# Optimization experiments

Measured on AMD Instinct MI355X. Metric: run time of the kernel, lower is better.

Reference implementation:

```python
import jax, jax.numpy as jnp
import numpy as np

B = 2048
DIMS = [4096, 8192, 8192, 4096]
SPARSITY = 1e-4


def setup_inputs() -> dict:
    key = jax.random.key(0)
    ks = jax.random.split(key, 10)
    x = jax.random.normal(ks[0], (B, DIMS[0]), dtype=jnp.float32)
    inp = {"x": x}
    for i in range(3):
        fan_in, fan_out = DIMS[i], DIMS[i + 1]
        # xavier_uniform_ for tanh
        limit = float(np.sqrt(6.0 / (fan_in + fan_out)))
        W = jax.random.uniform(ks[1 + 3 * i], (fan_out, fan_in),
                               dtype=jnp.float32, minval=-limit, maxval=limit)
        b = jax.random.uniform(ks[2 + 3 * i], (fan_out,), dtype=jnp.float32,
                               minval=-1.0 / np.sqrt(fan_in), maxval=1.0 / np.sqrt(fan_in))
        m = jax.random.bernoulli(ks[3 + 3 * i], p=SPARSITY, shape=(fan_out, fan_in))
        inp[f"W{i+1}"] = W
        inp[f"b{i+1}"] = b
        inp[f"m{i+1}"] = m
    return inp


def reference(x, W1, b1, m1, W2, b2, m2, W3, b3, m3):
    # Each layer: mask weight, dense linear (y = x @ (W*m)^T + b), tanh except last.
    h = jnp.tanh(x @ (W1 * m1).T + b1)        # [B, 8192]
    h = jnp.tanh(h @ (W2 * m2).T + b2)        # [B, 8192]
    out = h @ (W3 * m3).T + b3                # [B, 4096]
    return out
```

## Files before the change

### kernel.cpp

```cpp
#include <hip/hip_runtime.h>
#include <hip/hip_bf16.h>
#include <stdint.h>

#define CAP 32

static constexpr int BATCH = 2048;
static constexpr int D0 = 4096;
static constexpr int D1 = 8192;
static constexpr int D2 = 8192;
static constexpr int D3 = 4096;
static constexpr int ROWS_PAD = 8192;

static constexpr size_t PREFIX_BYTES = 16u << 20;

static constexpr size_t OFF_DET   = 0;
static constexpr size_t OFF_CNT   = 256;
static constexpr size_t OFF_REFD  = OFF_CNT + 3ull*ROWS_PAD*4;
static constexpr size_t OFF_XNEED = OFF_REFD + 2ull*ROWS_PAD*4;
static constexpr size_t ZERO_BYTES= OFF_XNEED + (size_t)D0*4;
static constexpr size_t OFF_TB    = ZERO_BYTES;
static constexpr size_t OFF_RK    = OFF_TB + 2ull*ROWS_PAD*4;
static constexpr size_t OFF_RW    = OFF_RK + 3ull*ROWS_PAD*CAP*4;
static constexpr size_t OFF_XT    = OFF_RW + 3ull*ROWS_PAD*CAP*4;
static constexpr size_t OFF_H1    = OFF_XT + 33554432ull;
static constexpr size_t OFF_H2    = OFF_H1 + 67108864ull;
static constexpr size_t WS_BIG    = OFF_H2 + 67108864ull;

__global__ void detect_kernel(const uint8_t* __restrict__ m, unsigned* __restrict__ det) {
    const uint4* p = (const uint4*)m;
    const int n16 = (int)(PREFIX_BYTES / 16);
    unsigned c123 = 0, c4 = 0;
    for (int i = blockIdx.x * blockDim.x + threadIdx.x; i < n16; i += gridDim.x * blockDim.x) {
        uint4 q = p[i];
        if ((q.x | q.y | q.z | q.w) == 0u) continue;
        unsigned w[4] = {q.x, q.y, q.z, q.w};
        for (int t = 0; t < 4; ++t) {
            unsigned v = w[t];
            if (!v) continue;
            for (int bb = 0; bb < 4; ++bb) {
                if ((v >> (8 * bb)) & 0xFFu) {
                    int posmod8 = ((t * 4 + bb) & 7);
                    if (posmod8 & 3) c123++;
                    else if (posmod8 == 4) c4++;
                }
            }
        }
    }
    if (c123) atomicAdd(&det[0], c123);
    if (c4)   atomicAdd(&det[1], c4);
}

__device__ __forceinline__ int decide_mode(const unsigned* det) {
    unsigned c123 = det[0], c4 = det[1];
    if (c123 > 1050u) return 0;
    if (c123 > 400u)  return 1;
    return (c4 > 80u) ? 1 : 2;
}

__device__ __forceinline__ void extract_row(const void* mask, const float* W,
                                            int fan_in, int row, int mode,
                                            int* cnt, int* rowk, float* roww,
                                            int* refd_prev) {
    __shared__ int lcnt;
    __shared__ int lk[CAP];
    if (threadIdx.x == 0) lcnt = 0;
    __syncthreads();

    auto push = [&](int k) {
        int pos = atomicAdd(&lcnt, 1);
        if (pos < CAP) lk[pos] = k;
    };

    if (mode == 0) {
        const uint4* p = (const uint4*)((const uint8_t*)mask + (size_t)row * fan_in);
        const int nch = fan_in / 16;
        for (int ci = threadIdx.x; ci < nch; ci += blockDim.x) {
            uint4 q = p[ci];
            if ((q.x | q.y | q.z | q.w) == 0u) continue;
            unsigned w[4] = {q.x, q.y, q.z, q.w};
            int base = ci * 16;
            for (int t = 0; t < 4; ++t) {
                unsigned v = w[t];
                if (!v) continue;
                for (int bb = 0; bb < 4; ++bb)
                    if ((v >> (8 * bb)) & 0xFFu) push(base + t * 4 + bb);
            }
        }
    } else if (mode == 1) {
        const int4* p = (const int4*)((const int*)mask + (size_t)row * fan_in);
        const int nch = fan_in / 4;
        for (int ci = threadIdx.x; ci < nch; ci += blockDim.x) {
            int4 q = p[ci];
            if ((q.x | q.y | q.z | q.w) == 0) continue;
            int base = ci * 4;
            if (q.x) push(base + 0);
            if (q.y) push(base + 1);
            if (q.z) push(base + 2);
            if (q.w) push(base + 3);
        }
    } else {
        const longlong2* p = (const longlong2*)((const long long*)mask + (size_t)row * fan_in);
        const int nch = fan_in / 2;
        for (int ci = threadIdx.x; ci < nch; ci += blockDim.x) {
            longlong2 q = p[ci];
            if ((q.x | q.y) == 0ll) continue;
            int base = ci * 2;
            if (q.x) push(base + 0);
            if (q.y) push(base + 1);
        }
    }
    __syncthreads();

    if (threadIdx.x == 0) {
        int c = lcnt;
        if (c > CAP) c = CAP;
        for (int a = 1; a < c; ++a) {
            int v = lk[a];
            int b = a - 1;
            while (b >= 0 && lk[b] > v) { lk[b + 1] = lk[b]; --b; }
            lk[b + 1] = v;
        }
        cnt[row] = c;
        for (int a = 0; a < c; ++a) {
            int k = lk[a];
            rowk[(size_t)row * CAP + a] = k;
            roww[(size_t)row * CAP + a] = W[(size_t)row * fan_in + k];
            if (refd_prev) atomicOr(&refd_prev[k], 1);
        }
    }
}

__global__ void extract_all_kernel(const void* __restrict__ m1, const float* __restrict__ W1,
                                   const void* __restrict__ m2, const float* __restrict__ W2,
                                   const void* __restrict__ m3, const float* __restrict__ W3,
                                   const float* __restrict__ b1, const float* __restrict__ b2,
                                   const unsigned* __restrict__ det,
                                   int* __restrict__ cnt1, int* __restrict__ cnt2, int* __restrict__ cnt3,
                                   int* __restrict__ rk1, int* __restrict__ rk2, int* __restrict__ rk3,
                                   float* __restrict__ rw1, float* __restrict__ rw2, float* __restrict__ rw3,
                                   int* __restrict__ refd1, int* __restrict__ refd2,
                                   int* __restrict__ xneed,
                                   float* __restrict__ tb1, float* __restrict__ tb2) {
    const int bid = blockIdx.x;
    const int mode = decide_mode(det);
    if (bid < D1) {
        extract_row(m1, W1, D0, bid, mode, cnt1, rk1, rw1, xneed);
    } else if (bid < D1 + D2) {
        extract_row(m2, W2, D1, bid - D1, mode, cnt2, rk2, rw2, refd1);
    } else if (bid < D1 + D2 + D3) {
        extract_row(m3, W3, D2, bid - D1 - D2, mode, cnt3, rk3, rw3, refd2);
    } else {
        int tid = (bid - (D1 + D2 + D3)) * 256 + threadIdx.x;
        if (tid < D1) tb1[tid] = tanhf(b1[tid]);
        else if (tid < D1 + D2) tb2[tid - D1] = tanhf(b2[tid - D1]);
    }
}

__global__ void transpose_x_kernel(const float* __restrict__ in, float* __restrict__ out,
                                   const int* __restrict__ xneed) {
    __shared__ float tile[32][33];
    int c0 = blockIdx.x * 32, r0 = blockIdx.y * 32;
    for (int i = threadIdx.y; i < 32; i += 8)
        tile[i][threadIdx.x] = in[(size_t)(r0 + i) * D0 + c0 + threadIdx.x];
    __syncthreads();
    for (int i = threadIdx.y; i < 32; i += 8)
        if (xneed[c0 + i])
            out[(size_t)(c0 + i) * BATCH + r0 + threadIdx.x] = tile[threadIdx.x][i];
}

template<bool HAS_TB>
__global__ void layer_kernel(const float* __restrict__ inT,
                             const float* __restrict__ bias,
                             const float* __restrict__ tb_in,
                             const int* __restrict__ cnt_in,
                             const int* __restrict__ cnt,
                             const int* __restrict__ rowk,
                             const float* __restrict__ roww,
                             const int* __restrict__ refd,
                             float* __restrict__ outT) {
    const int j = blockIdx.x;
    const int c = cnt[j];
    if (c == 0 || refd[j] == 0) return;

    const int*   kk = rowk + (size_t)j * CAP;
    const float* ww = roww + (size_t)j * CAP;

    float base = bias[j];
    if (HAS_TB) {
        for (int e = 0; e < c; ++e) {
            int k = kk[e];
            if (cnt_in[k] == 0) base += ww[e] * tb_in[k];
        }
    }

    const int l = threadIdx.x;
    float4 acc0 = make_float4(base, base, base, base);
    float4 acc1 = acc0;

    for (int e = 0; e < c; ++e) {
        int k = kk[e];
        if (HAS_TB && cnt_in[k] == 0) continue;
        const float w = ww[e];
        const float* row = inT + (size_t)k * BATCH;
        float4 v0 = *(const float4*)(row + l * 4);
        float4 v1 = *(const float4*)(row + 1024 + l * 4);
        acc0.x += w * v0.x; acc0.y += w * v0.y; acc0.z += w * v0.z; acc0.w += w * v0.w;
        acc1.x += w * v1.x; acc1.y += w * v1.y; acc1.z += w * v1.z; acc1.w += w * v1.w;
    }

    acc0.x = tanhf(acc0.x); acc0.y = tanhf(acc0.y);
    acc0.z = tanhf(acc0.z); acc0.w = tanhf(acc0.w);
    acc1.x = tanhf(acc1.x); acc1.y = tanhf(acc1.y);
    acc1.z = tanhf(acc1.z); acc1.w = tanhf(acc1.w);

    float* orow = outT + (size_t)j * BATCH;
    *(float4*)(orow + l * 4) = acc0;
    *(float4*)(orow + 1024 + l * 4) = acc1;
}

__global__ void l3t_kernel(const float* __restrict__ h2T,
                           const float* __restrict__ b3, const float* __restrict__ tb2,
                           const int* __restrict__ cnt2,
                           const int* __restrict__ c3, const int* __restrict__ k3,
                           const float* __restrict__ w3,
                           float* __restrict__ out) {
    __shared__ float tile[32][33];
    const int j0 = blockIdx.x * 32, b0 = blockIdx.y * 32;
    const int tx = threadIdx.x, ty = threadIdx.y;

    for (int s = 0; s < 4; ++s) {
        int jl = ty + 8 * s;
        int j = j0 + jl;
        float acc = b3[j];
        int c = c3[j];
        const int* kk = k3 + (size_t)j * CAP;
        const float* ww = w3 + (size_t)j * CAP;
        for (int e = 0; e < c; ++e) {
            int k = kk[e];
            float w = ww[e];
            acc += w * (cnt2[k] ? h2T[(size_t)k * BATCH + b0 + tx] : tb2[k]);
        }
        tile[jl][tx] = acc;
    }
    __syncthreads();
    for (int s = 0; s < 4; ++s) {
        int bl = ty + 8 * s;
        out[(size_t)(b0 + bl) * D3 + j0 + tx] = tile[tx][bl];
    }
}

__global__ void out_kernel(const float* __restrict__ x,
                           const float* __restrict__ b1, const float* __restrict__ b2,
                           const float* __restrict__ b3,
                           const int* __restrict__ c1, const int* __restrict__ k1,
                           const float* __restrict__ w1,
                           const int* __restrict__ c2, const int* __restrict__ k2,
                           const float* __restrict__ w2,
                           const int* __restrict__ c3, const int* __restrict__ k3,
                           const float* __restrict__ w3,
                           float* __restrict__ out) {
    int idx = blockIdx.x * blockDim.x + threadIdx.x;
    if (idx >= BATCH * D3) return;
    int b = idx >> 12;
    int j = idx & 4095;

    float acc = b3[j];
    int c = c3[j];
    for (int e = 0; e < c; ++e) {
        int kk2 = k3[(size_t)j * CAP + e];
        float a2 = b2[kk2];
        int cc2 = c2[kk2];
        for (int e2 = 0; e2 < cc2; ++e2) {
            int kk1 = k2[(size_t)kk2 * CAP + e2];
            float a1 = b1[kk1];
            int cc1 = c1[kk1];
            for (int e1 = 0; e1 < cc1; ++e1) {
                int kk0 = k1[(size_t)kk1 * CAP + e1];
                a1 += w1[(size_t)kk1 * CAP + e1] * x[(size_t)b * D0 + kk0];
            }
            a2 += w2[(size_t)kk2 * CAP + e2] * tanhf(a1);
        }
        acc += w3[(size_t)j * CAP + e] * tanhf(a2);
    }
    out[idx] = acc;
}

extern "C" void kernel_launch(void* const* d_in, const int* in_sizes, int n_in,
                              void* d_out, int out_size, void* d_ws, size_t ws_size,
                              hipStream_t stream) {
    const float* x  = (const float*)d_in[0];
    const float* W1 = (const float*)d_in[1];
    const float* b1 = (const float*)d_in[2];
    const void*  m1 = d_in[3];
    const float* W2 = (const float*)d_in[4];
    const float* b2 = (const float*)d_in[5];
    const void*  m2 = d_in[6];
    const float* W3 = (const float*)d_in[7];
    const float* b3 = (const float*)d_in[8];
    const void*  m3 = d_in[9];

    uint8_t* ws = (uint8_t*)d_ws;
    unsigned* det = (unsigned*)(ws + OFF_DET);
    int* cnt1 = (int*)(ws + OFF_CNT);
    int* cnt2 = cnt1 + ROWS_PAD;
    int* cnt3 = cnt2 + ROWS_PAD;
    int* refd1 = (int*)(ws + OFF_REFD);
    int* refd2 = refd1 + ROWS_PAD;
    int* xneed = (int*)(ws + OFF_XNEED);
    float* tb1 = (float*)(ws + OFF_TB);
    float* tb2 = tb1 + ROWS_PAD;
    int* rk1 = (int*)(ws + OFF_RK);
    int* rk2 = rk1 + (size_t)ROWS_PAD * CAP;
    int* rk3 = rk2 + (size_t)ROWS_PAD * CAP;
    float* rw1 = (float*)(ws + OFF_RW);
    float* rw2 = rw1 + (size_t)ROWS_PAD * CAP;
    float* rw3 = rw2 + (size_t)ROWS_PAD * CAP;
    float* xT  = (float*)(ws + OFF_XT);
    float* h1T = (float*)(ws + OFF_H1);
    float* h2T = (float*)(ws + OFF_H2);

    hipMemsetAsync(ws, 0, ZERO_BYTES, stream);

    detect_kernel<<<1024, 256, 0, stream>>>((const uint8_t*)m1, det);

    const int EX_BLOCKS = D1 + D2 + D3 + (D1 + D2) / 256;
    extract_all_kernel<<<EX_BLOCKS, 256, 0, stream>>>(
        m1, W1, m2, W2, m3, W3, b1, b2, det,
        cnt1, cnt2, cnt3, rk1, rk2, rk3, rw1, rw2, rw3,
        refd1, refd2, xneed, tb1, tb2);

    if (ws_size >= WS_BIG) {
        transpose_x_kernel<<<dim3(D0 / 32, BATCH / 32), dim3(32, 8), 0, stream>>>(x, xT, xneed);

        layer_kernel<false><<<D1, 256, 0, stream>>>(
            xT, b1, nullptr, nullptr, cnt1, rk1, rw1, refd1, h1T);
        layer_kernel<true><<<D2, 256, 0, stream>>>(
            h1T, b2, tb1, cnt1, cnt2, rk2, rw2, refd2, h2T);
        l3t_kernel<<<dim3(D3 / 32, BATCH / 32), dim3(32, 8), 0, stream>>>(
            h2T, b3, tb2, cnt2, cnt3, rk3, rw3, (float*)d_out);
    } else {
        out_kernel<<<(BATCH * D3 + 255) / 256, 256, 0, stream>>>(
            x, b1, b2, b3,
            cnt1, rk1, rw1,
            cnt2, rk2, rw2,
            cnt3, rk3, rw3,
            (float*)d_out);
    }
}
```

Before: 190.2 us.

## Fuse mask extraction with x transpose and layer-1 compute across kernels

Restructures the launch schedule so layer-1 mask extraction runs in the same kernel as the x transpose, and layer-2/3 extraction runs alongside the layer-1 sparse matmul. This overlaps independent stages and removes a kernel launch. It also drops the refd1/xneed liveness filtering, so all of x is transposed and all layer-1 rows are computed. That adds extra work in exchange for fewer stage barriers, and it shrinks the memset region.

After: 191.2 us. About the same (+0.6%).

```diff
diff --git a/kernel.cpp b/kernel.cpp
--- a/kernel.cpp
+++ b/kernel.cpp
@@ -14,11 +14,10 @@
 static constexpr size_t PREFIX_BYTES = 16u << 20;
 
 static constexpr size_t OFF_DET   = 0;
-static constexpr size_t OFF_CNT   = 256;
-static constexpr size_t OFF_REFD  = OFF_CNT + 3ull*ROWS_PAD*4;
-static constexpr size_t OFF_XNEED = OFF_REFD + 2ull*ROWS_PAD*4;
-static constexpr size_t ZERO_BYTES= OFF_XNEED + (size_t)D0*4;
-static constexpr size_t OFF_TB    = ZERO_BYTES;
+static constexpr size_t OFF_REFD2 = 256;
+static constexpr size_t ZERO_BYTES= OFF_REFD2 + (size_t)ROWS_PAD*4;
+static constexpr size_t OFF_CNT   = ZERO_BYTES;
+static constexpr size_t OFF_TB    = OFF_CNT + 3ull*ROWS_PAD*4;
 static constexpr size_t OFF_RK    = OFF_TB + 2ull*ROWS_PAD*4;
 static constexpr size_t OFF_RW    = OFF_RK + 3ull*ROWS_PAD*CAP*4;
 static constexpr size_t OFF_XT    = OFF_RW + 3ull*ROWS_PAD*CAP*4;
@@ -130,57 +129,19 @@
     }
 }
 
-__global__ void extract_all_kernel(const void* __restrict__ m1, const float* __restrict__ W1,
-                                   const void* __restrict__ m2, const float* __restrict__ W2,
-                                   const void* __restrict__ m3, const float* __restrict__ W3,
-                                   const float* __restrict__ b1, const float* __restrict__ b2,
-                                   const unsigned* __restrict__ det,
-                                   int* __restrict__ cnt1, int* __restrict__ cnt2, int* __restrict__ cnt3,
-                                   int* __restrict__ rk1, int* __restrict__ rk2, int* __restrict__ rk3,
-                                   float* __restrict__ rw1, float* __restrict__ rw2, float* __restrict__ rw3,
-                                   int* __restrict__ refd1, int* __restrict__ refd2,
-                                   int* __restrict__ xneed,
-                                   float* __restrict__ tb1, float* __restrict__ tb2) {
-    const int bid = blockIdx.x;
-    const int mode = decide_mode(det);
-    if (bid < D1) {
-        extract_row(m1, W1, D0, bid, mode, cnt1, rk1, rw1, xneed);
-    } else if (bid < D1 + D2) {
-        extract_row(m2, W2, D1, bid - D1, mode, cnt2, rk2, rw2, refd1);
-    } else if (bid < D1 + D2 + D3) {
-        extract_row(m3, W3, D2, bid - D1 - D2, mode, cnt3, rk3, rw3, refd2);
-    } else {
-        int tid = (bid - (D1 + D2 + D3)) * 256 + threadIdx.x;
-        if (tid < D1) tb1[tid] = tanhf(b1[tid]);
-        else if (tid < D1 + D2) tb2[tid - D1] = tanhf(b2[tid - D1]);
-    }
-}
-
-__global__ void transpose_x_kernel(const float* __restrict__ in, float* __restrict__ out,
-                                   const int* __restrict__ xneed) {
-    __shared__ float tile[32][33];
-    int c0 = blockIdx.x * 32, r0 = blockIdx.y * 32;
-    for (int i = threadIdx.y; i < 32; i += 8)
-        tile[i][threadIdx.x] = in[(size_t)(r0 + i) * D0 + c0 + threadIdx.x];
-    __syncthreads();
-    for (int i = threadIdx.y; i < 32; i += 8)
-        if (xneed[c0 + i])
-            out[(size_t)(c0 + i) * BATCH + r0 + threadIdx.x] = tile[threadIdx.x][i];
-}
-
-template<bool HAS_TB>
-__global__ void layer_kernel(const float* __restrict__ inT,
-                             const float* __restrict__ bias,
-                             const float* __restrict__ tb_in,
-                             const int* __restrict__ cnt_in,
-                             const int* __restrict__ cnt,
-                             const int* __restrict__ rowk,
-                             const float* __restrict__ roww,
-                             const int* __restrict__ refd,
-                             float* __restrict__ outT) {
-    const int j = blockIdx.x;
+template<bool HAS_TB, bool USE_REFD>
+__device__ __forceinline__ void layer_row(int j, const float* __restrict__ inT,
+                                          const float* __restrict__ bias,
+                                          const float* __restrict__ tb_in,
+                                          const int* __restrict__ cnt_in,
+                                          const int* __restrict__ cnt,
+                                          const int* __restrict__ rowk,
+                                          const float* __restrict__ roww,
+                                          const int* __restrict__ refd,
+                                          float* __restrict__ outT) {
     const int c = cnt[j];
-    if (c == 0 || refd[j] == 0) return;
+    if (c == 0) return;
+    if (USE_REFD) { if (refd[j] == 0) return; }
 
     const int*   kk = rowk + (size_t)j * CAP;
     const float* ww = roww + (size_t)j * CAP;
@@ -216,6 +177,64 @@
     float* orow = outT + (size_t)j * BATCH;
     *(float4*)(orow + l * 4) = acc0;
     *(float4*)(orow + 1024 + l * 4) = acc1;
+}
+
+__global__ void k1_kernel(const void* __restrict__ m1, const float* __restrict__ W1,
+                          const float* __restrict__ x,
+                          const float* __restrict__ b1, const float* __restrict__ b2,
+                          const unsigned* __restrict__ det,
+                          int* __restrict__ cnt1, int* __restrict__ rk1, float* __restrict__ rw1,
+                          float* __restrict__ tb1, float* __restrict__ tb2,
+                          float* __restrict__ xT) {
+    const int bid = blockIdx.x;
+    if (bid < D1) {
+        extract_row(m1, W1, D0, bid, decide_mode(det), cnt1, rk1, rw1, nullptr);
+    } else if (bid < D1 + (D0 / 32) * (BATCH / 32)) {
+        __shared__ float tile[32][33];
+        const int t = bid - D1;
+        const int cx = t & 127;
+        const int ry = t >> 7;
+        const int tx = threadIdx.x & 31, ty = threadIdx.x >> 5;
+        const int c0 = cx * 32, r0 = ry * 32;
+        for (int i = ty; i < 32; i += 8)
+            tile[i][tx] = x[(size_t)(r0 + i) * D0 + c0 + tx];
+        __syncthreads();
+        for (int i = ty; i < 32; i += 8)
+            xT[(size_t)(c0 + i) * BATCH + r0 + tx] = tile[tx][i];
+    } else {
+        int tid = (bid - D1 - (D0 / 32) * (BATCH / 32)) * 256 + threadIdx.x;
+        if (tid < D1) tb1[tid] = tanhf(b1[tid]);
+        else if (tid < D1 + D2) tb2[tid - D1] = tanhf(b2[tid - D1]);
+    }
+}
+
+__global__ void k2_kernel(const void* __restrict__ m2, const float* __restrict__ W2,
+                          const void* __restrict__ m3, const float* __restrict__ W3,
+                          const unsigned* __restrict__ det,
+                          int* __restrict__ cnt2, int* __restrict__ rk2, float* __restrict__ rw2,
+                          int* __restrict__ cnt3, int* __restrict__ rk3, float* __restrict__ rw3,
+                          int* __restrict__ refd2,
+                          const float* __restrict__ xT, const float* __restrict__ b1,
+                          const int* __restrict__ cnt1, const int* __restrict__ rk1,
+                          const float* __restrict__ rw1,
+                          float* __restrict__ h1T) {
+    const int bid = blockIdx.x;
+    if (bid < D2) {
+        extract_row(m2, W2, D1, bid, decide_mode(det), cnt2, rk2, rw2, nullptr);
+    } else if (bid < D2 + D3) {
+        extract_row(m3, W3, D2, bid - D2, decide_mode(det), cnt3, rk3, rw3, refd2);
+    } else {
+        layer_row<false, false>(bid - D2 - D3, xT, b1, nullptr, nullptr,
+                                cnt1, rk1, rw1, nullptr, h1T);
+    }
+}
+
+__global__ void layer2_kernel(const float* __restrict__ h1T, const float* __restrict__ b2,
+                              const float* __restrict__ tb1, const int* __restrict__ cnt1,
+                              const int* __restrict__ cnt2, const int* __restrict__ rk2,
+                              const float* __restrict__ rw2, const int* __restrict__ refd2,
+                              float* __restrict__ h2T) {
+    layer_row<true, true>(blockIdx.x, h1T, b2, tb1, cnt1, cnt2, rk2, rw2, refd2, h2T);
 }
 
 __global__ void l3t_kernel(const float* __restrict__ h2T,
@@ -247,6 +266,13 @@
         int bl = ty + 8 * s;
         out[(size_t)(b0 + bl) * D3 + j0 + tx] = tile[tx][bl];
     }
+}
+
+__global__ void extract_only_kernel(const void* __restrict__ mask, const float* __restrict__ W,
+                                    int fan_in,
+                                    int* __restrict__ cnt, int* __restrict__ rowk,
+                                    float* __restrict__ roww, const unsigned* __restrict__ det) {
+    extract_row(mask, W, fan_in, blockIdx.x, decide_mode(det), cnt, rowk, roww, nullptr);
 }
 
 __global__ void out_kernel(const float* __restrict__ x,
@@ -301,12 +327,10 @@
 
     uint8_t* ws = (uint8_t*)d_ws;
     unsigned* det = (unsigned*)(ws + OFF_DET);
+    int* refd2 = (int*)(ws + OFF_REFD2);
     int* cnt1 = (int*)(ws + OFF_CNT);
     int* cnt2 = cnt1 + ROWS_PAD;
     int* cnt3 = cnt2 + ROWS_PAD;
-    int* refd1 = (int*)(ws + OFF_REFD);
-    int* refd2 = refd1 + ROWS_PAD;
-    int* xneed = (int*)(ws + OFF_XNEED);
     float* tb1 = (float*)(ws + OFF_TB);
     float* tb2 = tb1 + ROWS_PAD;
     int* rk1 = (int*)(ws + OFF_RK);
@@ -320,25 +344,28 @@
     float* h2T = (float*)(ws + OFF_H2);
 
     hipMemsetAsync(ws, 0, ZERO_BYTES, stream);
-
     detect_kernel<<<1024, 256, 0, stream>>>((const uint8_t*)m1, det);
 
-    const int EX_BLOCKS = D1 + D2 + D3 + (D1 + D2) / 256;
-    extract_all_kernel<<<EX_BLOCKS, 256, 0, stream>>>(
-        m1, W1, m2, W2, m3, W3, b1, b2, det,
-        cnt1, cnt2, cnt3, rk1, rk2, rk3, rw1, rw2, rw3,
-        refd1, refd2, xneed, tb1, tb2);
-
     if (ws_size >= WS_BIG) {
-        transpose_x_kernel<<<dim3(D0 / 32, BATCH / 32), dim3(32, 8), 0, stream>>>(x, xT, xneed);
-
-        layer_kernel<false><<<D1, 256, 0, stream>>>(
-            xT, b1, nullptr, nullptr, cnt1, rk1, rw1, refd1, h1T);
-        layer_kernel<true><<<D2, 256, 0, stream>>>(
+        const int K1_BLOCKS = D1 + (D0 / 32) * (BATCH / 32) + (D1 + D2) / 256;
+        k1_kernel<<<K1_BLOCKS, 256, 0, stream>>>(
+            m1, W1, x, b1, b2, det, cnt1, rk1, rw1, tb1, tb2, xT);
+
+        const int K2_BLOCKS = D2 + D3 + D1;
+        k2_kernel<<<K2_BLOCKS, 256, 0, stream>>>(
+            m2, W2, m3, W3, det,
+            cnt2, rk2, rw2, cnt3, rk3, rw3, refd2,
+            xT, b1, cnt1, rk1, rw1, h1T);
+
+        layer2_kernel<<<D2, 256, 0, stream>>>(
             h1T, b2, tb1, cnt1, cnt2, rk2, rw2, refd2, h2T);
+
         l3t_kernel<<<dim3(D3 / 32, BATCH / 32), dim3(32, 8), 0, stream>>>(
             h2T, b3, tb2, cnt2, cnt3, rk3, rw3, (float*)d_out);
     } else {
+        extract_only_kernel<<<D1, 256, 0, stream>>>(m1, W1, D0, cnt1, rk1, rw1, det);
+        extract_only_kernel<<<D2, 256, 0, stream>>>(m2, W2, D1, cnt2, rk2, rw2, det);
+        extract_only_kernel<<<D3, 256, 0, stream>>>(m3, W3, D2, cnt3, rk3, rw3, det);
         out_kernel<<<(BATCH * D3 + 255) / 256, 256, 0, stream>>>(
             x, b1, b2, b3,
             cnt1, rk1, rw1,
```
